# Kernel optimization log

Hardware: AMD Instinct MI355X
Metric: run time of the kernel (lower is better)

## Reference

```python
import jax, jax.numpy as jnp
import numpy as np

N = 6144      # num_nodes
E = 256       # embed_dim
H = 4         # num_heads
D = E // H    # head_dim
EPS_LN = 1e-5


def setup_inputs() -> dict:
    key = jax.random.key(0)
    ks = jax.random.split(key, 8)
    x = jax.random.normal(ks[0], (N, E), jnp.float32)
    adj = (jax.random.uniform(ks[1], (N, N)) < 0.01).astype(jnp.float32)
    adj = jnp.maximum(adj, jnp.eye(N, dtype=jnp.float32))
    s = 1.0 / np.sqrt(E)
    Wq = jax.random.normal(ks[2], (E, E), jnp.float32) * s
    Wk = jax.random.normal(ks[3], (E, E), jnp.float32) * s
    Wv = jax.random.normal(ks[4], (E, E), jnp.float32) * s
    Wo = jax.random.normal(ks[5], (E, E), jnp.float32) * s
    bq = jnp.zeros((E,), jnp.float32)
    bk = jnp.zeros((E,), jnp.float32)
    bv = jnp.zeros((E,), jnp.float32)
    bo = jnp.zeros((E,), jnp.float32)
    gamma = jnp.ones((E,), jnp.float32)
    beta = jnp.zeros((E,), jnp.float32)
    return {"embeddings": x, "adj_matrix": adj,
            "Wq": Wq, "bq": bq, "Wk": Wk, "bk": bk, "Wv": Wv, "bv": bv,
            "Wo": Wo, "bo": bo, "gamma": gamma, "beta": beta}


def reference(embeddings, adj_matrix, Wq, bq, Wk, bk, Wv, bv, Wo, bo, gamma, beta):
    n, e = embeddings.shape
    h, d = H, e // H
    # linear projections (torch nn.Linear: x @ W.T + b)
    Q = (embeddings @ Wq.T + bq).reshape(n, h, d)
    K = (embeddings @ Wk.T + bk).reshape(n, h, d)
    V = (embeddings @ Wv.T + bv).reshape(n, h, d)
    # per-head node-node attention scores [h, n, n]
    scores = jnp.einsum('nhd,mhd->hnm', Q, K) / np.sqrt(d)
    scores = jnp.where(adj_matrix[None, :, :] == 0, -jnp.inf, scores)
    attn = jax.nn.softmax(scores, axis=-1)  # [h, n, n]
    out = jnp.einsum('hnm,mhd->nhd', attn, V).reshape(n, e)
    out = out @ Wo.T + bo
    # residual + LayerNorm
    y = embeddings + out
    mu = jnp.mean(y, axis=-1, keepdims=True)
    var = jnp.var(y, axis=-1, keepdims=True)
    return (y - mu) * jax.lax.rsqrt(var + EPS_LN) * gamma + beta
```

## Files before the change

### kernel.cpp

```cpp
#include <hip/hip_runtime.h>
#include <hip/hip_fp16.h>
#include <math.h>

constexpr int kN  = 6144;
constexpr int kE  = 256;
constexpr int kD  = 64;
constexpr int CAP = 128;

typedef float    f32x4  __attribute__((ext_vector_type(4)));
typedef _Float16 half8  __attribute__((ext_vector_type(8)));

__global__ __launch_bounds__(256) void convert_h(
    const float* __restrict__ X,
    const float* __restrict__ Wq, const float* __restrict__ Wk,
    const float* __restrict__ Wv, const float* __restrict__ Wo,
    __half* __restrict__ Xh,
    __half* __restrict__ Wqh, __half* __restrict__ Wkh,
    __half* __restrict__ Wvh, __half* __restrict__ Woh)
{
    const int i = blockIdx.x * 256 + threadIdx.x;
    const float* src; __half* dst; int off;
    if      (i < 393216) { src = X;  dst = Xh;  off = i; }
    else if (i < 409600) { src = Wq; dst = Wqh; off = i - 393216; }
    else if (i < 425984) { src = Wk; dst = Wkh; off = i - 409600; }
    else if (i < 442368) { src = Wv; dst = Wvh; off = i - 425984; }
    else                 { src = Wo; dst = Woh; off = i - 442368; }
    const float4 v = ((const float4*)src)[off];
    const __half2 a = __float22half2_rn(make_float2(v.x, v.y));
    const __half2 b = __float22half2_rn(make_float2(v.z, v.w));
    ((__half2*)dst)[off * 2 + 0] = a;
    ((__half2*)dst)[off * 2 + 1] = b;
}

template <int OUT_HALF>
__device__ __forceinline__ void gemm_mfma(
    const __half* __restrict__ A, const __half* __restrict__ B,
    const float* __restrict__ bias, const float* __restrict__ resid,
    void* __restrict__ Cout, const int n0, const int c0)
{
    const int lane = threadIdx.x & 63;
    const int w    = threadIdx.x >> 6;
    const int ar   = n0 + w * 16 + (lane & 15);
    const int ko   = (lane >> 4) * 8;

    f32x4 acc[4] = {{0.f,0.f,0.f,0.f},{0.f,0.f,0.f,0.f},
                    {0.f,0.f,0.f,0.f},{0.f,0.f,0.f,0.f}};

#pragma unroll
    for (int kc = 0; kc < kE; kc += 32) {
        const half8 af = *(const half8*)(A + (size_t)ar * kE + kc + ko);
#pragma unroll
        for (int j = 0; j < 4; ++j) {
            const int c = c0 + j * 16 + (lane & 15);
            const half8 bf = *(const half8*)(B + (size_t)c * kE + kc + ko);
            acc[j] = __builtin_amdgcn_mfma_f32_16x16x32_f16(af, bf, acc[j], 0, 0, 0);
        }
    }

    const int orow = n0 + w * 16 + (lane >> 4) * 4;
    const int ocol = lane & 15;
#pragma unroll
    for (int j = 0; j < 4; ++j) {
        const int c = c0 + j * 16 + ocol;
        const float bi = bias[c];
#pragma unroll
        for (int r = 0; r < 4; ++r) {
            float v = acc[j][r] + bi;
            if (resid) v += resid[(size_t)(orow + r) * kE + c];
            if (OUT_HALF) ((__half*)Cout)[(size_t)(orow + r) * kE + c] = __float2half(v);
            else          ((float*) Cout)[(size_t)(orow + r) * kE + c] = v;
        }
    }
}

__global__ __launch_bounds__(256) void proj_csr(
    const __half* __restrict__ Xh,
    const __half* __restrict__ Wqh, const float* __restrict__ bq,
    const __half* __restrict__ Wkh, const float* __restrict__ bk,
    const __half* __restrict__ Wvh, const float* __restrict__ bv,
    __half* __restrict__ Q, __half* __restrict__ K, __half* __restrict__ V,
    const float* __restrict__ adj,
    int* __restrict__ csr_cnt, int* __restrict__ csr_col)
{
    if (blockIdx.x < kN / 4) {
        const int lane = threadIdx.x & 63;
        const int r    = blockIdx.x * 4 + (threadIdx.x >> 6);
        const float* arow = adj + (size_t)r * kN;
        int* out = csr_col + (size_t)r * CAP;
        int base = 0;
#pragma unroll 4
        for (int it = 0; it < kN / 256; ++it) {
            const int col = it * 256 + lane * 4;
            const f32x4 a = __builtin_nontemporal_load((const f32x4*)(arow + col));
            const unsigned long long m0 = __ballot(a[0] != 0.f);
            const unsigned long long m1 = __ballot(a[1] != 0.f);
            const unsigned long long m2 = __ballot(a[2] != 0.f);
            const unsigned long long m3 = __ballot(a[3] != 0.f);
            const int c0 = __popcll(m0), c1 = __popcll(m1);
            const int c2 = __popcll(m2), c3 = __popcll(m3);
            const unsigned long long below = (1ull << lane) - 1ull;
            const int p0 = __popcll(m0 & below);
            const int p1 = c0 + __popcll(m1 & below);
            const int p2 = c0 + c1 + __popcll(m2 & below);
            const int p3 = c0 + c1 + c2 + __popcll(m3 & below);
            if (a[0] != 0.f && base + p0 < CAP) out[base + p0] = col + 0;
            if (a[1] != 0.f && base + p1 < CAP) out[base + p1] = col + 1;
            if (a[2] != 0.f && base + p2 < CAP) out[base + p2] = col + 2;
            if (a[3] != 0.f && base + p3 < CAP) out[base + p3] = col + 3;
            base += c0 + c1 + c2 + c3;
        }
        if (lane == 0) csr_cnt[r] = (base < CAP) ? base : CAP;
    } else {
        const int b = blockIdx.x - kN / 4;
        const int m = b / 384;
        const int r = b % 384;
        const int n0 = (r >> 2) * 64, c0 = (r & 3) * 64;
        if (m == 0)      gemm_mfma<1>(Xh, Wqh, bq, nullptr, Q, n0, c0);
        else if (m == 1) gemm_mfma<1>(Xh, Wkh, bk, nullptr, K, n0, c0);
        else             gemm_mfma<1>(Xh, Wvh, bv, nullptr, V, n0, c0);
    }
}

__global__ __launch_bounds__(256) void attn_csr(
    const int* __restrict__ csr_cnt, const int* __restrict__ csr_col,
    const __half* __restrict__ Qm,
    const __half* __restrict__ Km,
    const __half* __restrict__ Vm,
    __half* __restrict__ O)
{
    const int n    = blockIdx.x;
    const int t    = threadIdx.x;
    const int lane = t & 63;
    const int head = t >> 6;

    __shared__ int   nbr[CAP];
    __shared__ float q_lds[kE];
    __shared__ float p_lds[4][64];

    const int cnt = min(csr_cnt[n], CAP);
    if (t < CAP && t < cnt) nbr[t] = csr_col[(size_t)n * CAP + t];
    q_lds[t] = __half2float(Qm[(size_t)n * kE + t]);
    __syncthreads();

    float m = -INFINITY, lsum = 0.f, oacc = 0.f;
    const __half* Vh = Vm + head * kD;

    for (int b0 = 0; b0 < cnt; b0 += 64) {
        const int  bcnt  = min(64, cnt - b0);
        const bool valid = lane < bcnt;
        const int  idx   = valid ? nbr[b0 + lane] : n;
        const float4* krow = (const float4*)(Km + (size_t)idx * kE + head * kD);

        float s = 0.f;
#pragma unroll
        for (int i = 0; i < 8; ++i) {
            const float4 raw = krow[i];
            const __half2 h0 = *(const __half2*)&raw.x;
            const __half2 h1 = *(const __half2*)&raw.y;
            const __half2 h2 = *(const __half2*)&raw.z;
            const __half2 h3 = *(const __half2*)&raw.w;
            const float2 f0 = __half22float2(h0);
            const float2 f1 = __half22float2(h1);
            const float2 f2 = __half22float2(h2);
            const float2 f3 = __half22float2(h3);
            const float* qv = &q_lds[head * kD + i * 8];
            s += f0.x * qv[0] + f0.y * qv[1] + f1.x * qv[2] + f1.y * qv[3]
               + f2.x * qv[4] + f2.y * qv[5] + f3.x * qv[6] + f3.y * qv[7];
        }
        s *= 0.125f;
        if (!valid) s = -INFINITY;

        float bmax = s;
#pragma unroll
        for (int o = 32; o >= 1; o >>= 1) bmax = fmaxf(bmax, __shfl_xor(bmax, o, 64));
        const float mnew  = fmaxf(m, bmax);
        const float scale = __expf(m - mnew);
        const float p     = valid ? __expf(s - mnew) : 0.f;
        float bsum = p;
#pragma unroll
        for (int o = 32; o >= 1; o >>= 1) bsum += __shfl_xor(bsum, o, 64);
        lsum = lsum * scale + bsum;
        m    = mnew;
        oacc *= scale;

        p_lds[head][lane] = p;
        __syncthreads();

        int l = 0;
        for (; l + 8 <= bcnt; l += 8) {
            float pv[8], vv[8];
#pragma unroll
            for (int u = 0; u < 8; ++u) {
                const int vrow = nbr[b0 + l + u];
                vv[u] = __half2float(Vh[(size_t)vrow * kE + lane]);
                pv[u] = p_lds[head][l + u];
            }
#pragma unroll
            for (int u = 0; u < 8; ++u) oacc += pv[u] * vv[u];
        }
        for (; l < bcnt; ++l)
            oacc += p_lds[head][l] * __half2float(Vh[(size_t)nbr[b0 + l] * kE + lane]);
        __syncthreads();
    }

    O[(size_t)n * kE + head * kD + lane] = __float2half(oacc / lsum);
}

__global__ __launch_bounds__(256) void oproj(
    const __half* __restrict__ A, const __half* __restrict__ Woh,
    const float* __restrict__ bo, const float* __restrict__ X,
    float* __restrict__ Y)
{
    gemm_mfma<0>(A, Woh, bo, X, Y, blockIdx.x * 64, blockIdx.y * 64);
}

__global__ __launch_bounds__(256) void ln_rows(
    float* __restrict__ Y,
    const float* __restrict__ gamma, const float* __restrict__ beta)
{
    const int lane = threadIdx.x & 63;
    const int row  = blockIdx.x * 4 + (threadIdx.x >> 6);
    float4 v = *(const float4*)&Y[(size_t)row * kE + lane * 4];
    float ps = v.x + v.y + v.z + v.w;
    float pq = v.x * v.x + v.y * v.y + v.z * v.z + v.w * v.w;
#pragma unroll
    for (int o = 32; o >= 1; o >>= 1) {
        ps += __shfl_xor(ps, o, 64);
        pq += __shfl_xor(pq, o, 64);
    }
    const float mean = ps * (1.f / 256.f);
    const float var  = pq * (1.f / 256.f) - mean * mean;
    const float inv  = rsqrtf(var + 1e-5f);
    const float4 g  = *(const float4*)&gamma[lane * 4];
    const float4 be = *(const float4*)&beta[lane * 4];
    float4 o;
    o.x = (v.x - mean) * inv * g.x + be.x;
    o.y = (v.y - mean) * inv * g.y + be.y;
    o.z = (v.z - mean) * inv * g.z + be.z;
    o.w = (v.w - mean) * inv * g.w + be.w;
    *(float4*)&Y[(size_t)row * kE + lane * 4] = o;
}

extern "C" void kernel_launch(void* const* d_in, const int* in_sizes, int n_in,
                              void* d_out, int out_size, void* d_ws, size_t ws_size,
                              hipStream_t stream)
{
    const float* x   = (const float*)d_in[0];
    const float* adj = (const float*)d_in[1];
    const float* Wq  = (const float*)d_in[2];
    const float* bq  = (const float*)d_in[3];
    const float* Wk  = (const float*)d_in[4];
    const float* bk  = (const float*)d_in[5];
    const float* Wv  = (const float*)d_in[6];
    const float* bv  = (const float*)d_in[7];
    const float* Wo  = (const float*)d_in[8];
    const float* bo  = (const float*)d_in[9];
    const float* gam = (const float*)d_in[10];
    const float* bet = (const float*)d_in[11];

    char* p = (char*)d_ws;
    int*    csr_cnt = (int*)p;            p += (size_t)kN * 4;
    int*    csr_col = (int*)p;            p += (size_t)kN * CAP * 4;
    __half* Xh      = (__half*)p;         p += (size_t)kN * kE * 2;
    __half* Wqh     = (__half*)p;         p += (size_t)kE * kE * 2;
    __half* Wkh     = (__half*)p;         p += (size_t)kE * kE * 2;
    __half* Wvh     = (__half*)p;         p += (size_t)kE * kE * 2;
    __half* Woh     = (__half*)p;         p += (size_t)kE * kE * 2;
    __half* Q       = (__half*)p;         p += (size_t)kN * kE * 2;
    __half* K       = (__half*)p;         p += (size_t)kN * kE * 2;
    __half* V       = (__half*)p;         p += (size_t)kN * kE * 2;
    float*  Y       = (float*)d_out;

    convert_h<<<1792, 256, 0, stream>>>(x, Wq, Wk, Wv, Wo, Xh, Wqh, Wkh, Wvh, Woh);
    proj_csr<<<kN / 4 + 3 * (kN / 64) * (kE / 64), 256, 0, stream>>>(
        Xh, Wqh, bq, Wkh, bk, Wvh, bv, Q, K, V, adj, csr_cnt, csr_col);
    attn_csr<<<kN, 256, 0, stream>>>(csr_cnt, csr_col, Q, K, V, Q);
    dim3 go(kN / 64, kE / 64);
    oproj<<<go, 256, 0, stream>>>(Q, Woh, bo, x, Y);
    ln_rows<<<kN / 4, 256, 0, stream>>>(Y, gam, bet);
}
```

Measured before the change: 131.6 us.

## Fuse output projection with LayerNorm and drop block syncs in attention

The output projection and LayerNorm are merged into one kernel. Each 64-thread block computes full 16-row by 256-column tiles, so row statistics are reduced with shuffles and the intermediate fp32 Y never goes through global memory, and one launch is removed. The attention kernel gives each head its own copy of the neighbor list and query in LDS, which removes the __syncthreads barriers so the four wavefronts run independently. The cost is a small 384-block grid of single wavefronts with 16 accumulators each, which gives low occupancy and likely poor latency hiding on the fused GEMM.

```diff
diff --git a/kernel.cpp b/kernel.cpp
--- a/kernel.cpp
+++ b/kernel.cpp
@@ -32,11 +32,10 @@
     ((__half2*)dst)[off * 2 + 1] = b;
 }
 
-template <int OUT_HALF>
-__device__ __forceinline__ void gemm_mfma(
+__device__ __forceinline__ void gemm_mfma_h(
     const __half* __restrict__ A, const __half* __restrict__ B,
-    const float* __restrict__ bias, const float* __restrict__ resid,
-    void* __restrict__ Cout, const int n0, const int c0)
+    const float* __restrict__ bias, __half* __restrict__ Cout,
+    const int n0, const int c0)
 {
     const int lane = threadIdx.x & 63;
     const int w    = threadIdx.x >> 6;
@@ -64,12 +63,8 @@
         const int c = c0 + j * 16 + ocol;
         const float bi = bias[c];
 #pragma unroll
-        for (int r = 0; r < 4; ++r) {
-            float v = acc[j][r] + bi;
-            if (resid) v += resid[(size_t)(orow + r) * kE + c];
-            if (OUT_HALF) ((__half*)Cout)[(size_t)(orow + r) * kE + c] = __float2half(v);
-            else          ((float*) Cout)[(size_t)(orow + r) * kE + c] = v;
-        }
+        for (int r = 0; r < 4; ++r)
+            Cout[(size_t)(orow + r) * kE + c] = __float2half(acc[j][r] + bi);
     }
 }
 
@@ -115,9 +110,9 @@
         const int m = b / 384;
         const int r = b % 384;
         const int n0 = (r >> 2) * 64, c0 = (r & 3) * 64;
-        if (m == 0)      gemm_mfma<1>(Xh, Wqh, bq, nullptr, Q, n0, c0);
-        else if (m == 1) gemm_mfma<1>(Xh, Wkh, bk, nullptr, K, n0, c0);
-        else             gemm_mfma<1>(Xh, Wvh, bv, nullptr, V, n0, c0);
+        if (m == 0)      gemm_mfma_h(Xh, Wqh, bq, Q, n0, c0);
+        else if (m == 1) gemm_mfma_h(Xh, Wkh, bk, K, n0, c0);
+        else             gemm_mfma_h(Xh, Wvh, bv, V, n0, c0);
     }
 }
 
@@ -129,43 +124,40 @@
     __half* __restrict__ O)
 {
     const int n    = blockIdx.x;
-    const int t    = threadIdx.x;
-    const int lane = t & 63;
-    const int head = t >> 6;
-
-    __shared__ int   nbr[CAP];
-    __shared__ float q_lds[kE];
-    __shared__ float p_lds[4][64];
+    const int lane = threadIdx.x & 63;
+    const int head = threadIdx.x >> 6;
+
+    __shared__ int   nbr_s[4][CAP];
+    __shared__ float q_s[4][64];
+    __shared__ float p_s[4][64];
 
     const int cnt = min(csr_cnt[n], CAP);
-    if (t < CAP && t < cnt) nbr[t] = csr_col[(size_t)n * CAP + t];
-    q_lds[t] = __half2float(Qm[(size_t)n * kE + t]);
-    __syncthreads();
+    for (int i = lane; i < cnt; i += 64)
+        nbr_s[head][i] = csr_col[(size_t)n * CAP + i];
+    q_s[head][lane] = __half2float(Qm[(size_t)n * kE + head * kD + lane]);
 
     float m = -INFINITY, lsum = 0.f, oacc = 0.f;
     const __half* Vh = Vm + head * kD;
+    const float4* qv4 = (const float4*)&q_s[head][0];
 
     for (int b0 = 0; b0 < cnt; b0 += 64) {
         const int  bcnt  = min(64, cnt - b0);
         const bool valid = lane < bcnt;
-        const int  idx   = valid ? nbr[b0 + lane] : n;
+        const int  idx   = valid ? nbr_s[head][b0 + lane] : n;
         const float4* krow = (const float4*)(Km + (size_t)idx * kE + head * kD);
 
         float s = 0.f;
 #pragma unroll
         for (int i = 0; i < 8; ++i) {
             const float4 raw = krow[i];
-            const __half2 h0 = *(const __half2*)&raw.x;
-            const __half2 h1 = *(const __half2*)&raw.y;
-            const __half2 h2 = *(const __half2*)&raw.z;
-            const __half2 h3 = *(const __half2*)&raw.w;
-            const float2 f0 = __half22float2(h0);
-            const float2 f1 = __half22float2(h1);
-            const float2 f2 = __half22float2(h2);
-            const float2 f3 = __half22float2(h3);
-            const float* qv = &q_lds[head * kD + i * 8];
-            s += f0.x * qv[0] + f0.y * qv[1] + f1.x * qv[2] + f1.y * qv[3]
-               + f2.x * qv[4] + f2.y * qv[5] + f3.x * qv[6] + f3.y * qv[7];
+            const float2 f0 = __half22float2(*(const __half2*)&raw.x);
+            const float2 f1 = __half22float2(*(const __half2*)&raw.y);
+            const float2 f2 = __half22float2(*(const __half2*)&raw.z);
+            const float2 f3 = __half22float2(*(const __half2*)&raw.w);
+            const float4 qa = qv4[i * 2 + 0];
+            const float4 qb = qv4[i * 2 + 1];
+            s += f0.x * qa.x + f0.y * qa.y + f1.x * qa.z + f1.y * qa.w
+               + f2.x * qb.x + f2.y * qb.y + f3.x * qb.z + f3.y * qb.w;
         }
         s *= 0.125f;
         if (!valid) s = -INFINITY;
@@ -183,62 +175,90 @@
         m    = mnew;
         oacc *= scale;
 
-        p_lds[head][lane] = p;
-        __syncthreads();
+        p_s[head][lane] = p;
 
         int l = 0;
         for (; l + 8 <= bcnt; l += 8) {
             float pv[8], vv[8];
 #pragma unroll
             for (int u = 0; u < 8; ++u) {
-                const int vrow = nbr[b0 + l + u];
+                const int vrow = nbr_s[head][b0 + l + u];
                 vv[u] = __half2float(Vh[(size_t)vrow * kE + lane]);
-                pv[u] = p_lds[head][l + u];
+                pv[u] = p_s[head][l + u];
             }
 #pragma unroll
             for (int u = 0; u < 8; ++u) oacc += pv[u] * vv[u];
         }
         for (; l < bcnt; ++l)
-            oacc += p_lds[head][l] * __half2float(Vh[(size_t)nbr[b0 + l] * kE + lane]);
-        __syncthreads();
+            oacc += p_s[head][l] * __half2float(Vh[(size_t)nbr_s[head][b0 + l] * kE + lane]);
     }
 
     O[(size_t)n * kE + head * kD + lane] = __float2half(oacc / lsum);
 }
 
-__global__ __launch_bounds__(256) void oproj(
+__global__ __launch_bounds__(64) void oproj_ln(
     const __half* __restrict__ A, const __half* __restrict__ Woh,
     const float* __restrict__ bo, const float* __restrict__ X,
-    float* __restrict__ Y)
-{
-    gemm_mfma<0>(A, Woh, bo, X, Y, blockIdx.x * 64, blockIdx.y * 64);
-}
-
-__global__ __launch_bounds__(256) void ln_rows(
-    float* __restrict__ Y,
-    const float* __restrict__ gamma, const float* __restrict__ beta)
-{
-    const int lane = threadIdx.x & 63;
-    const int row  = blockIdx.x * 4 + (threadIdx.x >> 6);
-    float4 v = *(const float4*)&Y[(size_t)row * kE + lane * 4];
-    float ps = v.x + v.y + v.z + v.w;
-    float pq = v.x * v.x + v.y * v.y + v.z * v.z + v.w * v.w;
-#pragma unroll
-    for (int o = 32; o >= 1; o >>= 1) {
-        ps += __shfl_xor(ps, o, 64);
-        pq += __shfl_xor(pq, o, 64);
-    }
-    const float mean = ps * (1.f / 256.f);
-    const float var  = pq * (1.f / 256.f) - mean * mean;
-    const float inv  = rsqrtf(var + 1e-5f);
-    const float4 g  = *(const float4*)&gamma[lane * 4];
-    const float4 be = *(const float4*)&beta[lane * 4];
-    float4 o;
-    o.x = (v.x - mean) * inv * g.x + be.x;
-    o.y = (v.y - mean) * inv * g.y + be.y;
-    o.z = (v.z - mean) * inv * g.z + be.z;
-    o.w = (v.w - mean) * inv * g.w + be.w;
-    *(float4*)&Y[(size_t)row * kE + lane * 4] = o;
+    const float* __restrict__ gamma, const float* __restrict__ beta,
+    float* __restrict__ Out)
+{
+    const int n0   = blockIdx.x * 16;
+    const int lane = threadIdx.x;
+    const int ar   = n0 + (lane & 15);
+    const int ko   = (lane >> 4) * 8;
+
+    f32x4 acc[16];
+#pragma unroll
+    for (int j = 0; j < 16; ++j) acc[j] = (f32x4){0.f, 0.f, 0.f, 0.f};
+
+#pragma unroll
+    for (int kc = 0; kc < kE; kc += 32) {
+        const half8 af = *(const half8*)(A + (size_t)ar * kE + kc + ko);
+#pragma unroll
+        for (int j = 0; j < 16; ++j) {
+            const int c = j * 16 + (lane & 15);
+            const half8 bf = *(const half8*)(Woh + (size_t)c * kE + kc + ko);
+            acc[j] = __builtin_amdgcn_mfma_f32_16x16x32_f16(af, bf, acc[j], 0, 0, 0);
+        }
+    }
+
+    const int orow = n0 + (lane >> 4) * 4;
+    const int ocol = lane & 15;
+
+#pragma unroll
+    for (int j = 0; j < 16; ++j) {
+        const int c = j * 16 + ocol;
+        const float bi = bo[c];
+#pragma unroll
+        for (int r = 0; r < 4; ++r)
+            acc[j][r] += bi + X[(size_t)(orow + r) * kE + c];
+    }
+
+    float mean[4], inv[4];
+#pragma unroll
+    for (int r = 0; r < 4; ++r) {
+        float s = 0.f, q = 0.f;
+#pragma unroll
+        for (int j = 0; j < 16; ++j) { s += acc[j][r]; q += acc[j][r] * acc[j][r]; }
+#pragma unroll
+        for (int o = 8; o >= 1; o >>= 1) {
+            s += __shfl_xor(s, o, 64);
+            q += __shfl_xor(q, o, 64);
+        }
+        mean[r] = s * (1.f / 256.f);
+        const float var = q * (1.f / 256.f) - mean[r] * mean[r];
+        inv[r] = rsqrtf(var + 1e-5f);
+    }
+
+#pragma unroll
+    for (int j = 0; j < 16; ++j) {
+        const int c = j * 16 + ocol;
+        const float g  = gamma[c];
+        const float be = beta[c];
+#pragma unroll
+        for (int r = 0; r < 4; ++r)
+            Out[(size_t)(orow + r) * kE + c] = (acc[j][r] - mean[r]) * inv[r] * g + be;
+    }
 }
 
 extern "C" void kernel_launch(void* const* d_in, const int* in_sizes, int n_in,
@@ -275,7 +295,5 @@
     proj_csr<<<kN / 4 + 3 * (kN / 64) * (kE / 64), 256, 0, stream>>>(
         Xh, Wqh, bq, Wkh, bk, Wvh, bv, Q, K, V, adj, csr_cnt, csr_col);
     attn_csr<<<kN, 256, 0, stream>>>(csr_cnt, csr_col, Q, K, V, Q);
-    dim3 go(kN / 64, kE / 64);
-    oproj<<<go, 256, 0, stream>>>(Q, Woh, bo, x, Y);
-    ln_rows<<<kN / 4, 256, 0, stream>>>(Y, gam, bet);
-}
+    oproj_ln<<<kN / 16, 64, 0, stream>>>(Q, Woh, bo, x, gam, bet, Y);
+}
```

Result: slower. 140.8 us (+6.9%).
